# Kernel tuning notes

Measured on AMD Instinct MI355X. Metric: run time of the kernel, lower is better.

Reference implementation:

```python
import jax, jax.numpy as jnp
import numpy as np
from jax import lax

STRIDE = 1
PAD = 1


def setup_inputs() -> dict:
    key = jax.random.key(0)
    k1, k2 = jax.random.split(key)
    X = jax.random.normal(k1, (16, 64, 256, 256), dtype=jnp.float32)
    K = jax.random.normal(k2, (3, 3), dtype=jnp.float32)
    return {"X": X, "K": K}


def reference(X, K):
    # out[b, c, i, j] = sum(patch(X[b, c], i, j) * K)
    # == depthwise conv with a single shared 2D kernel for all channels.
    B, C, H, W = X.shape
    x = X.reshape(B * C, 1, H, W)            # fold channels into batch
    k = K[None, None, :, :]                  # [O=1, I=1, kh, kw]
    out = lax.conv_general_dilated(
        x, k,
        window_strides=(STRIDE, STRIDE),
        padding=[(PAD, PAD), (PAD, PAD)],
        dimension_numbers=("NCHW", "OIHW", "NCHW"),
    )
    Ho, Wo = out.shape[2], out.shape[3]
    return out.reshape(B, C, Ho, Wo)
```

## Files before the change

### kernel.cpp

```cpp
#include <hip/hip_runtime.h>


#define CONV_H 256
#define CONV_W 256
#define CONV_W4 64
#define NPLANES (16 * 64)
#define ROWS_PER_THREAD 16
#define STRIPES (CONV_H / ROWS_PER_THREAD)

typedef float v4f __attribute__((ext_vector_type(4)));

struct Row { float4 c; float l, r; };

__device__ __forceinline__ Row load_row(const float* __restrict__ rowp, int lane) {
    Row v;
    v.c = *(const float4*)rowp;
    float l = __shfl_up(v.c.w, 1);
    float r = __shfl_down(v.c.x, 1);
    v.l = (lane == 0)  ? 0.f : l;
    v.r = (lane == 63) ? 0.f : r;
    return v;
}

__device__ __forceinline__ Row zero_row() {
    Row v;
    v.c = make_float4(0.f, 0.f, 0.f, 0.f);
    v.l = 0.f; v.r = 0.f;
    return v;
}

__global__ __launch_bounds__(256)
void conv3x3_kernel(const float* __restrict__ X,
                    const float* __restrict__ Kw,
                    float* __restrict__ out)
{
    const float k00 = Kw[0], k01 = Kw[1], k02 = Kw[2];
    const float k10 = Kw[3], k11 = Kw[4], k12 = Kw[5];
    const float k20 = Kw[6], k21 = Kw[7], k22 = Kw[8];

    const int chunk = gridDim.x >> 3;
    const int lb = (blockIdx.x & 7) * chunk + (blockIdx.x >> 3);

    const int tid    = lb * blockDim.x + threadIdx.x;
    const int lane   = threadIdx.x & 63;
    const int w4     = tid & (CONV_W4 - 1);
    const int stripe = tid >> 6;
    const int h0     = (stripe & (STRIPES - 1)) << 4;
    const int p      = stripe >> 4;

    const float* plane = X + (size_t)p * (CONV_H * CONV_W);
    const int col0 = w4 << 2;
    float* outp = out + (size_t)p * (CONV_H * CONV_W) + (size_t)h0 * CONV_W + col0;

    Row rm = (h0 > 0) ? load_row(plane + (h0 - 1) * CONV_W + col0, lane) : zero_row();
    Row rc = load_row(plane + h0 * CONV_W + col0, lane);

    #pragma unroll
    for (int i = 0; i < ROWS_PER_THREAD; ++i) {
        const int hp = h0 + i + 1;
        Row rp = (hp < CONV_H) ? load_row(plane + hp * CONV_W + col0, lane)
                               : zero_row();

        float4 o;
        o.x = k00 * rm.l   + k01 * rm.c.x + k02 * rm.c.y
            + k10 * rc.l   + k11 * rc.c.x + k12 * rc.c.y
            + k20 * rp.l   + k21 * rp.c.x + k22 * rp.c.y;
        o.y = k00 * rm.c.x + k01 * rm.c.y + k02 * rm.c.z
            + k10 * rc.c.x + k11 * rc.c.y + k12 * rc.c.z
            + k20 * rp.c.x + k21 * rp.c.y + k22 * rp.c.z;
        o.z = k00 * rm.c.y + k01 * rm.c.z + k02 * rm.c.w
            + k10 * rc.c.y + k11 * rc.c.z + k12 * rc.c.w
            + k20 * rp.c.y + k21 * rp.c.z + k22 * rp.c.w;
        o.w = k00 * rm.c.z + k01 * rm.c.w + k02 * rm.r
            + k10 * rc.c.z + k11 * rc.c.w + k12 * rc.r
            + k20 * rp.c.z + k21 * rp.c.w + k22 * rp.r;

        v4f ov = { o.x, o.y, o.z, o.w };
        __builtin_nontemporal_store(ov, (v4f*)(outp + i * CONV_W));

        rm = rc;
        rc = rp;
    }
}

extern "C" void kernel_launch(void* const* d_in, const int* in_sizes, int n_in,
                              void* d_out, int out_size, void* d_ws, size_t ws_size,
                              hipStream_t stream) {
    const float* X  = (const float*)d_in[0];
    const float* Kw = (const float*)d_in[1];
    float* out = (float*)d_out;

    const int total_threads = NPLANES * STRIPES * CONV_W4;
    const int block = 256;
    const int grid = total_threads / block;
    conv3x3_kernel<<<grid, block, 0, stream>>>(X, Kw, out);
}
```

Measured before the change: 454.0 us.

## Halve rows per thread and software-pipeline row loads with a ring buffer

Cuts rows per thread from 16 to 8, doubling the thread count, and keeps a 4-deep ring of raw float4 row loads issued ahead of use. Out-of-range rows become clamped loads masked by multiplying with zero, instead of branching. The aim is more memory parallelism and better latency hiding in a bandwidth-bound stencil. The cost is more halo re-reads per stripe and extra multiplies for masking.

```diff
diff --git a/kernel.cpp b/kernel.cpp
--- a/kernel.cpp
+++ b/kernel.cpp
@@ -5,27 +5,24 @@
 #define CONV_W 256
 #define CONV_W4 64
 #define NPLANES (16 * 64)
-#define ROWS_PER_THREAD 16
+#define ROWS_PER_THREAD 8
 #define STRIPES (CONV_H / ROWS_PER_THREAD)
+#define PDEPTH 4
 
 typedef float v4f __attribute__((ext_vector_type(4)));
 
 struct Row { float4 c; float l, r; };
 
-__device__ __forceinline__ Row load_row(const float* __restrict__ rowp, int lane) {
+__device__ __forceinline__ Row expand_row(float4 c, int lane, float valid) {
     Row v;
-    v.c = *(const float4*)rowp;
-    float l = __shfl_up(v.c.w, 1);
-    float r = __shfl_down(v.c.x, 1);
-    v.l = (lane == 0)  ? 0.f : l;
-    v.r = (lane == 63) ? 0.f : r;
-    return v;
-}
-
-__device__ __forceinline__ Row zero_row() {
-    Row v;
-    v.c = make_float4(0.f, 0.f, 0.f, 0.f);
-    v.l = 0.f; v.r = 0.f;
+    float l = __shfl_up(c.w, 1);
+    float r = __shfl_down(c.x, 1);
+    v.c.x = c.x * valid;
+    v.c.y = c.y * valid;
+    v.c.z = c.z * valid;
+    v.c.w = c.w * valid;
+    v.l = (lane == 0)  ? 0.f : l * valid;
+    v.r = (lane == 63) ? 0.f : r * valid;
     return v;
 }
 
@@ -45,21 +42,35 @@
     const int lane   = threadIdx.x & 63;
     const int w4     = tid & (CONV_W4 - 1);
     const int stripe = tid >> 6;
-    const int h0     = (stripe & (STRIPES - 1)) << 4;
-    const int p      = stripe >> 4;
+    const int h0     = (stripe & (STRIPES - 1)) << 3;
+    const int p      = stripe >> 5;
 
-    const float* plane = X + (size_t)p * (CONV_H * CONV_W);
-    const int col0 = w4 << 2;
-    float* outp = out + (size_t)p * (CONV_H * CONV_W) + (size_t)h0 * CONV_W + col0;
+    const float* colp = X + (size_t)p * (CONV_H * CONV_W) + (w4 << 2);
+    float* outp = out + (size_t)p * (CONV_H * CONV_W)
+                      + (size_t)h0 * CONV_W + (w4 << 2);
 
-    Row rm = (h0 > 0) ? load_row(plane + (h0 - 1) * CONV_W + col0, lane) : zero_row();
-    Row rc = load_row(plane + h0 * CONV_W + col0, lane);
+    float4 raw[PDEPTH];
+    #pragma unroll
+    for (int j = 0; j < PDEPTH; ++j) {
+        int r   = h0 - 1 + j;
+        int rcl = min(max(r, 0), CONV_H - 1);
+        raw[j] = *(const float4*)(colp + rcl * CONV_W);
+    }
+
+    Row rm = expand_row(raw[0], lane, (h0 > 0) ? 1.f : 0.f);
+    Row rc = expand_row(raw[1], lane, 1.f);
 
     #pragma unroll
     for (int i = 0; i < ROWS_PER_THREAD; ++i) {
-        const int hp = h0 + i + 1;
-        Row rp = (hp < CONV_H) ? load_row(plane + hp * CONV_W + col0, lane)
-                               : zero_row();
+        if (i < ROWS_PER_THREAD - 2) {
+            int r   = h0 + PDEPTH - 1 + i;
+            int rcl = min(r, CONV_H - 1);
+            raw[i & (PDEPTH - 1)] = *(const float4*)(colp + rcl * CONV_W);
+        }
+
+        const int rpr = h0 + 1 + i;
+        Row rp = expand_row(raw[(i + 2) & (PDEPTH - 1)], lane,
+                            (rpr < CONV_H) ? 1.f : 0.f);
 
         float4 o;
         o.x = k00 * rm.l   + k01 * rm.c.x + k02 * rm.c.y
```

After: 442.7 us. -2.5%, faster.
